# Performance work log

Hardware: AMD Instinct MI355X
Metric: run time of the kernel (lower is better)

The kernel has to match this reference:

```python
import jax, jax.numpy as jnp
import numpy as np

N_TOTAL = 200000
DIM = 256
N_GRAPHS = 8192
N_ITERS = 6


def setup_inputs() -> dict:
    key = jax.random.key(0)
    k1, k2, k3, k4, k5, k6 = jax.random.split(key, 6)
    x = jax.random.normal(k1, (N_TOTAL, DIM), dtype=jnp.float32)
    batch = jnp.sort(jax.random.randint(k2, (N_TOTAL,), 0, N_GRAPHS)).astype(jnp.int32)
    bound = 1.0 / np.sqrt(DIM)
    W_ih = jax.random.uniform(k3, (4 * DIM, DIM), jnp.float32, -bound, bound)
    W_hh = jax.random.uniform(k4, (4 * DIM, DIM), jnp.float32, -bound, bound)
    b_ih = jax.random.uniform(k5, (4 * DIM,), jnp.float32, -bound, bound)
    b_hh = jax.random.uniform(k6, (4 * DIM,), jnp.float32, -bound, bound)
    return {"x": x, "batch": batch, "n_graphs": N_GRAPHS,
            "W_ih": W_ih, "W_hh": W_hh, "b_ih": b_ih, "b_hh": b_hh}


def _lstm_cell(inp, h, c, W_ih, W_hh, b_ih, b_hh):
    # PyTorch LSTMCell: gates ordered i, f, g, o
    gates = inp @ W_ih.T + b_ih + h @ W_hh.T + b_hh
    i, f, g, o = jnp.split(gates, 4, axis=-1)
    c_new = jax.nn.sigmoid(f) * c + jax.nn.sigmoid(i) * jnp.tanh(g)
    h_new = jax.nn.sigmoid(o) * jnp.tanh(c_new)
    return h_new, c_new


def reference(x, batch, n_graphs, W_ih, W_hh, b_ih, b_hh):
    dim = x.shape[1]
    h = jnp.zeros((n_graphs, dim), x.dtype)
    c = jnp.zeros((n_graphs, dim), x.dtype)
    readout = jnp.zeros((n_graphs, dim), x.dtype)
    for _ in range(N_ITERS):
        # attention scores per node: <x_v, q_{g(v)}>
        scores = jnp.sum(x * h[batch], axis=-1)  # (N,)
        # torch scatter_reduce_ amax with zero init includes the 0 -> max(seg_max, 0)
        seg_max = jax.ops.segment_max(scores, batch, num_segments=n_graphs,
                                      indices_are_sorted=True)
        seg_max = jnp.maximum(seg_max, 0.0)
        e = jnp.exp(scores - seg_max[batch])
        seg_sum = jax.ops.segment_sum(e, batch, num_segments=n_graphs,
                                      indices_are_sorted=True)
        w = e / (seg_sum[batch] + 1e-8)  # (N,)
        readout = jax.ops.segment_sum(x * w[:, None], batch, num_segments=n_graphs,
                                      indices_are_sorted=True)  # (G, dim)
        h, c = _lstm_cell(readout, h, c, W_ih, W_hh, b_ih, b_hh)
    return jnp.concatenate([h, readout], axis=-1)  # (G, 2*dim)
```

## Files before the change

### kernel.cpp

```cpp
#include <hip/hip_runtime.h>
#include <hip/hip_bf16.h>
#include <hip/hip_fp16.h>
#include <stdint.h>

#define DIM 256
#define NG 8192
#define KDIM 512
#define GDIM 1024
#define N_ITERS 6
#define CHUNK 32

#define BM 128
#define BN 128
#define BK 64

typedef __hip_bfloat16 bf16;
typedef __attribute__((ext_vector_type(8))) short bf16x8;
typedef __attribute__((ext_vector_type(4))) float f32x4;
typedef __attribute__((ext_vector_type(8))) unsigned short u16x8;
typedef __attribute__((ext_vector_type(4))) unsigned short u16x4;

__device__ __forceinline__ void async16(void* lds, const void* g) {
    __builtin_amdgcn_global_load_lds((const __attribute__((address_space(1))) void*)g,
                                     (__attribute__((address_space(3))) void*)lds, 16, 0, 0);
}
__device__ __forceinline__ float fast_sigmoid(float v) {
    return 1.0f / (1.0f + __expf(-v));
}
__device__ __forceinline__ float fast_tanh(float v) {
    float e = __expf(2.0f * v);
    return (e - 1.0f) / (e + 1.0f);
}
__device__ __forceinline__ unsigned short f2bf(float v) {
    __hip_bfloat16 t = __float2bfloat16(v);
    unsigned short u; __builtin_memcpy(&u, &t, 2); return u;
}
__device__ __forceinline__ unsigned short f2h(float v) {
    __half t = __float2half_rn(v);
    unsigned short u; __builtin_memcpy(&u, &t, 2); return u;
}
__device__ __forceinline__ float h2f(unsigned short u) {
    __half t; __builtin_memcpy(&t, &u, 2);
    return __half2float(t);
}

__global__ void k_offsets(const int* __restrict__ batch, int* __restrict__ offs, int n_nodes) {
    int v = blockIdx.x * blockDim.x + threadIdx.x;
    if (v >= n_nodes) return;
    int b = batch[v];
    int bp = (v == 0) ? -1 : batch[v - 1];
    for (int g = bp + 1; g <= b; ++g) offs[g] = v;
    if (v == n_nodes - 1) {
        for (int g = b + 1; g <= NG; ++g) offs[g] = n_nodes;
    }
}

__global__ void k_prep_w(const float* __restrict__ Wih, const float* __restrict__ Whh,
                         const float* __restrict__ bih, const float* __restrict__ bhh,
                         bf16* __restrict__ Wcat, float* __restrict__ bsum) {
    int idx = blockIdx.x * blockDim.x + threadIdx.x;
    if (idx < GDIM * KDIM) {
        int n = idx >> 9;
        int k = idx & (KDIM - 1);
        int d = n >> 2, gate = n & 3;
        int j = gate * DIM + d;
        float v = (k < DIM) ? Wih[j * DIM + k] : Whh[j * DIM + (k - DIM)];
        Wcat[idx] = __float2bfloat16(v);
    }
    if (idx < GDIM) {
        int d = idx >> 2, gate = idx & 3;
        int j = gate * DIM + d;
        bsum[idx] = bih[j] + bhh[j];
    }
}

__global__ void k_zero(float* __restrict__ h, float* __restrict__ c, bf16* __restrict__ Acat0) {
    int i = blockIdx.x * blockDim.x + threadIdx.x;
    if (i >= NG * DIM) return;
    h[i] = 0.0f; c[i] = 0.0f;
    Acat0[(size_t)(i >> 8) * KDIM + DIM + (i & 255)] = __float2bfloat16(0.0f);
}

template <bool FIRST>
__global__ __launch_bounds__(256) void k_att(const float* __restrict__ xf,
                                             unsigned short* __restrict__ xb,
                                             const float* __restrict__ h,
                                             const int* __restrict__ offs,
                                             float* __restrict__ readout,
                                             bf16* __restrict__ AcatOut) {
    const int g = blockIdx.x;
    const int tid = threadIdx.x;
    const int wave = tid >> 6, lane = tid & 63;
    const int sub = lane >> 5, hl = lane & 31;

    __shared__ unsigned short xs[CHUNK][DIM];
    __shared__ float sc[CHUNK];
    __shared__ float esh[CHUNK];

    float hreg[8];
    {
        const float4 h0 = *(const float4*)&h[(size_t)g * DIM + hl * 8];
        const float4 h1 = *(const float4*)&h[(size_t)g * DIM + hl * 8 + 4];
        hreg[0] = h0.x; hreg[1] = h0.y; hreg[2] = h0.z; hreg[3] = h0.w;
        hreg[4] = h1.x; hreg[5] = h1.y; hreg[6] = h1.z; hreg[7] = h1.w;
    }

    const int start = offs[g], end = offs[g + 1];
    float racc = 0.0f;
    float m = 0.0f;
    float s = 0.0f;

    for (int base = start; base < end; base += CHUNK) {
        const int cnt = min(CHUNK, end - base);
        for (int i = wave * 2; i < cnt; i += 8) {
            const int r = i + sub;
            if (r < cnt) {
                u16x8 pk;
                float dt = 0.0f;
                if (FIRST) {
                    const float4 a = *(const float4*)&xf[(size_t)(base + r) * DIM + hl * 8];
                    const float4 b = *(const float4*)&xf[(size_t)(base + r) * DIM + hl * 8 + 4];
                    float xv[8] = {a.x, a.y, a.z, a.w, b.x, b.y, b.z, b.w};
                    #pragma unroll
                    for (int j = 0; j < 8; ++j) { pk[j] = f2h(xv[j]); dt = fmaf(xv[j], hreg[j], dt); }
                    *(u16x8*)&xb[(size_t)(base + r) * DIM + hl * 8] = pk;
                } else {
                    pk = *(const u16x8*)&xb[(size_t)(base + r) * DIM + hl * 8];
                    #pragma unroll
                    for (int j = 0; j < 8; ++j) dt = fmaf(h2f(pk[j]), hreg[j], dt);
                }
                *(u16x8*)&xs[r][hl * 8] = pk;
                #pragma unroll
                for (int off = 16; off > 0; off >>= 1) dt += __shfl_xor(dt, off);
                if (hl == 0) sc[r] = dt;
            }
        }
        __syncthreads();
        float cmax = m;
        for (int i = 0; i < cnt; ++i) cmax = fmaxf(cmax, sc[i]);
        const float alpha = __expf(m - cmax);
        racc *= alpha;
        s *= alpha;
        if (tid < cnt) esh[tid] = __expf(sc[tid] - cmax);
        m = cmax;
        __syncthreads();
        for (int i = 0; i < cnt; ++i) {
            const float e = esh[i];
            s += e;
            racc = fmaf(e, h2f(xs[i][tid]), racc);
        }
        __syncthreads();
    }

    const float out = racc / (s + 1e-8f);
    readout[(size_t)g * DIM + tid] = out;
    AcatOut[(size_t)g * KDIM + tid] = __float2bfloat16(out);
}

__global__ __launch_bounds__(256) void k_gemm_cell(const bf16* __restrict__ A,
                                                   const bf16* __restrict__ W,
                                                   const float* __restrict__ bsum,
                                                   float* __restrict__ cst,
                                                   float* __restrict__ hst,
                                                   bf16* __restrict__ AcatN) {
    __shared__ union {
        struct { bf16 As[BM * BK]; bf16 Bs[BN * BK]; } st;
        float ep[32][132];
    } sm;

    const int tid = threadIdx.x;
    const int wave = tid >> 6, lane = tid & 63;
    const int m0 = blockIdx.x * BM;
    const int n0 = blockIdx.y * BN;
    const int wr = wave >> 1, wc = wave & 1;

    f32x4 acc[4][4] = {};

    const int chunk = lane & 7;

    for (int k0 = 0; k0 < KDIM; k0 += BK) {
        #pragma unroll
        for (int i = 0; i < 4; ++i) {
            const int grp = wave * 32 + i * 8;
            async16(&sm.st.As[grp * BK],
                    A + (size_t)(m0 + grp + (lane >> 3)) * KDIM + k0 + chunk * 8);
        }
        #pragma unroll
        for (int i = 0; i < 4; ++i) {
            const int grp = wave * 32 + i * 8;
            async16(&sm.st.Bs[grp * BK],
                    W + (size_t)(n0 + grp + (lane >> 3)) * KDIM + k0 + chunk * 8);
        }
        asm volatile("s_waitcnt vmcnt(0)" ::: "memory");
        __syncthreads();

        #pragma unroll
        for (int ks = 0; ks < BK; ks += 32) {
            bf16x8 a[4], b[4];
            #pragma unroll
            for (int mi = 0; mi < 4; ++mi)
                a[mi] = *(const bf16x8*)&sm.st.As[(wr * 64 + mi * 16 + (lane & 15)) * BK + ks + (lane >> 4) * 8];
            #pragma unroll
            for (int ni = 0; ni < 4; ++ni)
                b[ni] = *(const bf16x8*)&sm.st.Bs[(wc * 64 + ni * 16 + (lane & 15)) * BK + ks + (lane >> 4) * 8];
            #pragma unroll
            for (int mi = 0; mi < 4; ++mi)
                #pragma unroll
                for (int ni = 0; ni < 4; ++ni)
                    acc[mi][ni] = __builtin_amdgcn_mfma_f32_16x16x32_bf16(a[mi], b[ni], acc[mi][ni], 0, 0, 0);
        }
        __syncthreads();
    }

    float bv[4];
    #pragma unroll
    for (int ni = 0; ni < 4; ++ni)
        bv[ni] = bsum[n0 + wc * 64 + ni * 16 + (lane & 15)];

    const int d0 = n0 >> 2;
    const int lr = tid >> 3;
    const int dd = (tid & 7) * 4;

    #pragma unroll
    for (int mi = 0; mi < 4; ++mi) {
        __syncthreads();
        #pragma unroll
        for (int ni = 0; ni < 4; ++ni) {
            const int colL = wc * 64 + ni * 16 + (lane & 15);
            #pragma unroll
            for (int r = 0; r < 4; ++r) {
                const int lrow = wr * 16 + (lane >> 4) * 4 + r;
                sm.ep[lrow][colL] = acc[mi][ni][r] + bv[ni];
            }
        }
        __syncthreads();
        const int grow = m0 + (lr >> 4) * 64 + mi * 16 + (lr & 15);
        const int d = d0 + dd;
        float co[4], cn[4], hn[4];
        *(float4*)co = *(const float4*)&cst[(size_t)grow * DIM + d];
        u16x4 hb;
        #pragma unroll
        for (int j = 0; j < 4; ++j) {
            const float4 q = *(const float4*)&sm.ep[lr][(dd + j) * 4];
            cn[j] = fast_sigmoid(q.y) * co[j] + fast_sigmoid(q.x) * fast_tanh(q.z);
            hn[j] = fast_sigmoid(q.w) * fast_tanh(cn[j]);
            hb[j] = f2bf(hn[j]);
        }
        *(float4*)&cst[(size_t)grow * DIM + d] = *(float4*)cn;
        *(float4*)&hst[(size_t)grow * DIM + d] = *(float4*)hn;
        *(u16x4*)&AcatN[(size_t)grow * KDIM + DIM + d] = hb;
    }
}

__global__ void k_out(const float* __restrict__ h, const float* __restrict__ readout,
                      float* __restrict__ out) {
    int idx = blockIdx.x * blockDim.x + threadIdx.x;
    if (idx >= NG * KDIM) return;
    const int g = idx >> 9, d = idx & (KDIM - 1);
    out[idx] = (d < DIM) ? h[(size_t)g * DIM + d] : readout[(size_t)g * DIM + (d - DIM)];
}

extern "C" void kernel_launch(void* const* d_in, const int* in_sizes, int n_in,
                              void* d_out, int out_size, void* d_ws, size_t ws_size,
                              hipStream_t stream) {
    const float* x     = (const float*)d_in[0];
    const int*   batch = (const int*)d_in[1];
    const float* Wih   = (const float*)d_in[3];
    const float* Whh   = (const float*)d_in[4];
    const float* bih   = (const float*)d_in[5];
    const float* bhh   = (const float*)d_in[6];
    const int n_nodes  = in_sizes[0] / DIM;
    float* out = (float*)d_out;

    char* ws = (char*)d_ws;
    size_t off = 0;
    auto alloc = [&](size_t bytes) -> void* {
        off = (off + 255) & ~(size_t)255;
        void* p = ws + off;
        off += bytes;
        return p;
    };
    int*   offs    = (int*)  alloc((size_t)(NG + 1) * sizeof(int));
    bf16*  Wcat    = (bf16*) alloc((size_t)GDIM * KDIM * sizeof(bf16));
    float* bsum    = (float*)alloc((size_t)GDIM * sizeof(float));
    bf16*  Acat0   = (bf16*) alloc((size_t)NG * KDIM * sizeof(bf16));
    bf16*  Acat1   = (bf16*) alloc((size_t)NG * KDIM * sizeof(bf16));
    float* h       = (float*)alloc((size_t)NG * DIM * sizeof(float));
    float* c       = (float*)alloc((size_t)NG * DIM * sizeof(float));
    float* readout = (float*)alloc((size_t)NG * DIM * sizeof(float));
    unsigned short* xb = (unsigned short*)alloc((size_t)n_nodes * DIM * sizeof(unsigned short));
    (void)ws_size; (void)n_in; (void)out_size;

    k_offsets<<<(n_nodes + 255) / 256, 256, 0, stream>>>(batch, offs, n_nodes);
    k_prep_w<<<(GDIM * KDIM + 255) / 256, 256, 0, stream>>>(Wih, Whh, bih, bhh, Wcat, bsum);
    k_zero<<<(NG * DIM + 255) / 256, 256, 0, stream>>>(h, c, Acat0);

    for (int it = 0; it < N_ITERS; ++it) {
        bf16* Ain  = (it & 1) ? Acat1 : Acat0;
        bf16* Aout = (it & 1) ? Acat0 : Acat1;
        if (it == 0)
            k_att<true><<<NG, 256, 0, stream>>>(x, xb, h, offs, readout, Ain);
        else
            k_att<false><<<NG, 256, 0, stream>>>(x, xb, h, offs, readout, Ain);
        k_gemm_cell<<<dim3(NG / BM, GDIM / BN), 256, 0, stream>>>(Ain, Wcat, bsum, c, h, Aout);
    }
    k_out<<<(NG * KDIM + 255) / 256, 256, 0, stream>>>(h, readout, out);
}
```

Before: 883.9 us.

## Use one wave per graph with online softmax and fuse setup/output kernels

The attention kernel now assigns one wavefront per graph instead of a 256-thread block. Each half-wave processes alternate nodes with a streaming online softmax kept in registers, then the two halves merge with cross-lane shuffles. This removes the shared-memory staging and the block barriers. The three setup kernels are merged into one, and the final iteration writes h and readout straight into the output so the separate concat kernel goes away. The per-wave loop is serial over nodes, so graphs with many nodes could load-balance less well.

Result: faster. 832.5 us (-5.8%).

```diff
diff --git a/kernel.cpp b/kernel.cpp
--- a/kernel.cpp
+++ b/kernel.cpp
@@ -8,7 +8,6 @@
 #define KDIM 512
 #define GDIM 1024
 #define N_ITERS 6
-#define CHUNK 32
 
 #define BM 128
 #define BN 128
@@ -44,125 +43,132 @@
     return __half2float(t);
 }
 
-__global__ void k_offsets(const int* __restrict__ batch, int* __restrict__ offs, int n_nodes) {
-    int v = blockIdx.x * blockDim.x + threadIdx.x;
-    if (v >= n_nodes) return;
-    int b = batch[v];
-    int bp = (v == 0) ? -1 : batch[v - 1];
-    for (int g = bp + 1; g <= b; ++g) offs[g] = v;
-    if (v == n_nodes - 1) {
-        for (int g = b + 1; g <= NG; ++g) offs[g] = n_nodes;
-    }
-}
-
-__global__ void k_prep_w(const float* __restrict__ Wih, const float* __restrict__ Whh,
-                         const float* __restrict__ bih, const float* __restrict__ bhh,
-                         bf16* __restrict__ Wcat, float* __restrict__ bsum) {
-    int idx = blockIdx.x * blockDim.x + threadIdx.x;
+__global__ void k_prep(const int* __restrict__ batch, int n_nodes, int* __restrict__ offs,
+                       const float* __restrict__ Wih, const float* __restrict__ Whh,
+                       const float* __restrict__ bih, const float* __restrict__ bhh,
+                       bf16* __restrict__ Wcat, float* __restrict__ bsum,
+                       float* __restrict__ h, float* __restrict__ c, bf16* __restrict__ Acat0) {
+    const int idx = blockIdx.x * blockDim.x + threadIdx.x;
+    if (idx < NG * DIM) {
+        h[idx] = 0.0f; c[idx] = 0.0f;
+        Acat0[(size_t)(idx >> 8) * KDIM + DIM + (idx & 255)] = __float2bfloat16(0.0f);
+    }
     if (idx < GDIM * KDIM) {
-        int n = idx >> 9;
-        int k = idx & (KDIM - 1);
-        int d = n >> 2, gate = n & 3;
-        int j = gate * DIM + d;
-        float v = (k < DIM) ? Wih[j * DIM + k] : Whh[j * DIM + (k - DIM)];
+        const int n = idx >> 9;
+        const int k = idx & (KDIM - 1);
+        const int d = n >> 2, gate = n & 3;
+        const int j = gate * DIM + d;
+        const float v = (k < DIM) ? Wih[j * DIM + k] : Whh[j * DIM + (k - DIM)];
         Wcat[idx] = __float2bfloat16(v);
     }
     if (idx < GDIM) {
-        int d = idx >> 2, gate = idx & 3;
-        int j = gate * DIM + d;
+        const int d = idx >> 2, gate = idx & 3;
+        const int j = gate * DIM + d;
         bsum[idx] = bih[j] + bhh[j];
     }
-}
-
-__global__ void k_zero(float* __restrict__ h, float* __restrict__ c, bf16* __restrict__ Acat0) {
-    int i = blockIdx.x * blockDim.x + threadIdx.x;
-    if (i >= NG * DIM) return;
-    h[i] = 0.0f; c[i] = 0.0f;
-    Acat0[(size_t)(i >> 8) * KDIM + DIM + (i & 255)] = __float2bfloat16(0.0f);
-}
-
-template <bool FIRST>
+    if (idx < n_nodes) {
+        const int b = batch[idx];
+        const int bp = (idx == 0) ? -1 : batch[idx - 1];
+        for (int g = bp + 1; g <= b; ++g) offs[g] = idx;
+        if (idx == n_nodes - 1)
+            for (int g = b + 1; g <= NG; ++g) offs[g] = n_nodes;
+    }
+}
+
+template <bool FIRST, bool LAST>
 __global__ __launch_bounds__(256) void k_att(const float* __restrict__ xf,
                                              unsigned short* __restrict__ xb,
                                              const float* __restrict__ h,
                                              const int* __restrict__ offs,
-                                             float* __restrict__ readout,
+                                             float* __restrict__ rout,
                                              bf16* __restrict__ AcatOut) {
-    const int g = blockIdx.x;
-    const int tid = threadIdx.x;
-    const int wave = tid >> 6, lane = tid & 63;
-    const int sub = lane >> 5, hl = lane & 31;
-
-    __shared__ unsigned short xs[CHUNK][DIM];
-    __shared__ float sc[CHUNK];
-    __shared__ float esh[CHUNK];
+    const int wave = threadIdx.x >> 6;
+    const int g = (blockIdx.x << 2) + wave;
+    const int lane = threadIdx.x & 63;
+    const int half = lane >> 5, hl = lane & 31;
 
     float hreg[8];
     {
-        const float4 h0 = *(const float4*)&h[(size_t)g * DIM + hl * 8];
-        const float4 h1 = *(const float4*)&h[(size_t)g * DIM + hl * 8 + 4];
-        hreg[0] = h0.x; hreg[1] = h0.y; hreg[2] = h0.z; hreg[3] = h0.w;
-        hreg[4] = h1.x; hreg[5] = h1.y; hreg[6] = h1.z; hreg[7] = h1.w;
+        const float4 a = *(const float4*)&h[(size_t)g * DIM + hl * 8];
+        const float4 b = *(const float4*)&h[(size_t)g * DIM + hl * 8 + 4];
+        hreg[0] = a.x; hreg[1] = a.y; hreg[2] = a.z; hreg[3] = a.w;
+        hreg[4] = b.x; hreg[5] = b.y; hreg[6] = b.z; hreg[7] = b.w;
     }
 
     const int start = offs[g], end = offs[g + 1];
-    float racc = 0.0f;
+    float racc[8] = {0, 0, 0, 0, 0, 0, 0, 0};
     float m = 0.0f;
     float s = 0.0f;
 
-    for (int base = start; base < end; base += CHUNK) {
-        const int cnt = min(CHUNK, end - base);
-        for (int i = wave * 2; i < cnt; i += 8) {
-            const int r = i + sub;
-            if (r < cnt) {
+    for (int r0 = start; r0 < end; r0 += 2) {
+        const int r = r0 + half;
+        const bool valid = (r < end);
+        float xv[8];
+        float dt = 0.0f;
+        if (valid) {
+            if (FIRST) {
+                const float4 a = *(const float4*)&xf[(size_t)r * DIM + hl * 8];
+                const float4 b = *(const float4*)&xf[(size_t)r * DIM + hl * 8 + 4];
+                xv[0] = a.x; xv[1] = a.y; xv[2] = a.z; xv[3] = a.w;
+                xv[4] = b.x; xv[5] = b.y; xv[6] = b.z; xv[7] = b.w;
                 u16x8 pk;
-                float dt = 0.0f;
-                if (FIRST) {
-                    const float4 a = *(const float4*)&xf[(size_t)(base + r) * DIM + hl * 8];
-                    const float4 b = *(const float4*)&xf[(size_t)(base + r) * DIM + hl * 8 + 4];
-                    float xv[8] = {a.x, a.y, a.z, a.w, b.x, b.y, b.z, b.w};
-                    #pragma unroll
-                    for (int j = 0; j < 8; ++j) { pk[j] = f2h(xv[j]); dt = fmaf(xv[j], hreg[j], dt); }
-                    *(u16x8*)&xb[(size_t)(base + r) * DIM + hl * 8] = pk;
-                } else {
-                    pk = *(const u16x8*)&xb[(size_t)(base + r) * DIM + hl * 8];
-                    #pragma unroll
-                    for (int j = 0; j < 8; ++j) dt = fmaf(h2f(pk[j]), hreg[j], dt);
-                }
-                *(u16x8*)&xs[r][hl * 8] = pk;
                 #pragma unroll
-                for (int off = 16; off > 0; off >>= 1) dt += __shfl_xor(dt, off);
-                if (hl == 0) sc[r] = dt;
+                for (int j = 0; j < 8; ++j) pk[j] = f2h(xv[j]);
+                *(u16x8*)&xb[(size_t)r * DIM + hl * 8] = pk;
+            } else {
+                const u16x8 pk = *(const u16x8*)&xb[(size_t)r * DIM + hl * 8];
+                #pragma unroll
+                for (int j = 0; j < 8; ++j) xv[j] = h2f(pk[j]);
             }
-        }
-        __syncthreads();
-        float cmax = m;
-        for (int i = 0; i < cnt; ++i) cmax = fmaxf(cmax, sc[i]);
-        const float alpha = __expf(m - cmax);
-        racc *= alpha;
-        s *= alpha;
-        if (tid < cnt) esh[tid] = __expf(sc[tid] - cmax);
-        m = cmax;
-        __syncthreads();
-        for (int i = 0; i < cnt; ++i) {
-            const float e = esh[i];
-            s += e;
-            racc = fmaf(e, h2f(xs[i][tid]), racc);
-        }
-        __syncthreads();
-    }
-
-    const float out = racc / (s + 1e-8f);
-    readout[(size_t)g * DIM + tid] = out;
-    AcatOut[(size_t)g * KDIM + tid] = __float2bfloat16(out);
-}
-
+            #pragma unroll
+            for (int j = 0; j < 8; ++j) dt = fmaf(xv[j], hreg[j], dt);
+        }
+        #pragma unroll
+        for (int off = 16; off > 0; off >>= 1) dt += __shfl_xor(dt, off);
+        if (valid) {
+            const float mn = fmaxf(m, dt);
+            const float al = __expf(m - mn);
+            const float e  = __expf(dt - mn);
+            s = s * al + e;
+            #pragma unroll
+            for (int j = 0; j < 8; ++j) racc[j] = fmaf(racc[j], al, e * xv[j]);
+            m = mn;
+        }
+    }
+
+    const float mo = __shfl_xor(m, 32);
+    const float M  = fmaxf(m, mo);
+    const float al = __expf(m - M);
+    s *= al;
+    #pragma unroll
+    for (int j = 0; j < 8; ++j) racc[j] *= al;
+    s += __shfl_xor(s, 32);
+    #pragma unroll
+    for (int j = 0; j < 8; ++j) racc[j] += __shfl_xor(racc[j], 32);
+    const float inv = 1.0f / (s + 1e-8f);
+    float o[8];
+    #pragma unroll
+    for (int j = 0; j < 8; ++j) o[j] = racc[j] * inv;
+
+    if (half == 0) {
+        u16x8 pk;
+        #pragma unroll
+        for (int j = 0; j < 8; ++j) pk[j] = f2bf(o[j]);
+        *(u16x8*)&AcatOut[(size_t)g * KDIM + hl * 8] = pk;
+    } else if (LAST) {
+        *(float4*)&rout[(size_t)g * KDIM + hl * 8]     = make_float4(o[0], o[1], o[2], o[3]);
+        *(float4*)&rout[(size_t)g * KDIM + hl * 8 + 4] = make_float4(o[4], o[5], o[6], o[7]);
+    }
+}
+
+template <bool LAST>
 __global__ __launch_bounds__(256) void k_gemm_cell(const bf16* __restrict__ A,
                                                    const bf16* __restrict__ W,
                                                    const float* __restrict__ bsum,
                                                    float* __restrict__ cst,
                                                    float* __restrict__ hst,
-                                                   bf16* __restrict__ AcatN) {
+                                                   bf16* __restrict__ AcatN,
+                                                   float* __restrict__ hout) {
     __shared__ union {
         struct { bf16 As[BM * BK]; bf16 Bs[BN * BK]; } st;
         float ep[32][132];
@@ -175,7 +181,6 @@
     const int wr = wave >> 1, wc = wave & 1;
 
     f32x4 acc[4][4] = {};
-
     const int chunk = lane & 7;
 
     for (int k0 = 0; k0 < KDIM; k0 += BK) {
@@ -246,18 +251,14 @@
             hn[j] = fast_sigmoid(q.w) * fast_tanh(cn[j]);
             hb[j] = f2bf(hn[j]);
         }
-        *(float4*)&cst[(size_t)grow * DIM + d] = *(float4*)cn;
-        *(float4*)&hst[(size_t)grow * DIM + d] = *(float4*)hn;
-        *(u16x4*)&AcatN[(size_t)grow * KDIM + DIM + d] = hb;
-    }
-}
-
-__global__ void k_out(const float* __restrict__ h, const float* __restrict__ readout,
-                      float* __restrict__ out) {
-    int idx = blockIdx.x * blockDim.x + threadIdx.x;
-    if (idx >= NG * KDIM) return;
-    const int g = idx >> 9, d = idx & (KDIM - 1);
-    out[idx] = (d < DIM) ? h[(size_t)g * DIM + d] : readout[(size_t)g * DIM + (d - DIM)];
+        if (LAST) {
+            *(float4*)&hout[(size_t)grow * KDIM + d] = *(float4*)hn;
+        } else {
+            *(float4*)&cst[(size_t)grow * DIM + d] = *(float4*)cn;
+            *(float4*)&hst[(size_t)grow * DIM + d] = *(float4*)hn;
+            *(u16x4*)&AcatN[(size_t)grow * KDIM + DIM + d] = hb;
+        }
+    }
 }
 
 extern "C" void kernel_launch(void* const* d_in, const int* in_sizes, int n_in,
@@ -280,29 +281,34 @@
         off += bytes;
         return p;
     };
-    int*   offs    = (int*)  alloc((size_t)(NG + 1) * sizeof(int));
-    bf16*  Wcat    = (bf16*) alloc((size_t)GDIM * KDIM * sizeof(bf16));
-    float* bsum    = (float*)alloc((size_t)GDIM * sizeof(float));
-    bf16*  Acat0   = (bf16*) alloc((size_t)NG * KDIM * sizeof(bf16));
-    bf16*  Acat1   = (bf16*) alloc((size_t)NG * KDIM * sizeof(bf16));
-    float* h       = (float*)alloc((size_t)NG * DIM * sizeof(float));
-    float* c       = (float*)alloc((size_t)NG * DIM * sizeof(float));
-    float* readout = (float*)alloc((size_t)NG * DIM * sizeof(float));
+    int*   offs  = (int*)  alloc((size_t)(NG + 1) * sizeof(int));
+    bf16*  Wcat  = (bf16*) alloc((size_t)GDIM * KDIM * sizeof(bf16));
+    float* bsum  = (float*)alloc((size_t)GDIM * sizeof(float));
+    bf16*  Acat0 = (bf16*) alloc((size_t)NG * KDIM * sizeof(bf16));
+    bf16*  Acat1 = (bf16*) alloc((size_t)NG * KDIM * sizeof(bf16));
+    float* h     = (float*)alloc((size_t)NG * DIM * sizeof(float));
+    float* c     = (float*)alloc((size_t)NG * DIM * sizeof(float));
     unsigned short* xb = (unsigned short*)alloc((size_t)n_nodes * DIM * sizeof(unsigned short));
     (void)ws_size; (void)n_in; (void)out_size;
 
-    k_offsets<<<(n_nodes + 255) / 256, 256, 0, stream>>>(batch, offs, n_nodes);
-    k_prep_w<<<(GDIM * KDIM + 255) / 256, 256, 0, stream>>>(Wih, Whh, bih, bhh, Wcat, bsum);
-    k_zero<<<(NG * DIM + 255) / 256, 256, 0, stream>>>(h, c, Acat0);
+    k_prep<<<NG * DIM / 256, 256, 0, stream>>>(batch, n_nodes, offs, Wih, Whh, bih, bhh,
+                                               Wcat, bsum, h, c, Acat0);
 
     for (int it = 0; it < N_ITERS; ++it) {
         bf16* Ain  = (it & 1) ? Acat1 : Acat0;
         bf16* Aout = (it & 1) ? Acat0 : Acat1;
         if (it == 0)
-            k_att<true><<<NG, 256, 0, stream>>>(x, xb, h, offs, readout, Ain);
+            k_att<true, false><<<NG / 4, 256, 0, stream>>>(x, xb, h, offs, nullptr, Ain);
+        else if (it < N_ITERS - 1)
+            k_att<false, false><<<NG / 4, 256, 0, stream>>>(x, xb, h, offs, nullptr, Ain);
         else
-            k_att<false><<<NG, 256, 0, stream>>>(x, xb, h, offs, readout, Ain);
-        k_gemm_cell<<<dim3(NG / BM, GDIM / BN), 256, 0, stream>>>(Ain, Wcat, bsum, c, h, Aout);
-    }
-    k_out<<<(NG * KDIM + 255) / 256, 256, 0, stream>>>(h, readout, out);
-}
+            k_att<false, true><<<NG / 4, 256, 0, stream>>>(x, xb, h, offs, out + DIM, Ain);
+
+        if (it < N_ITERS - 1)
+            k_gemm_cell<false><<<dim3(NG / BM, GDIM / BN), 256, 0, stream>>>(
+                Ain, Wcat, bsum, c, h, Aout, nullptr);
+        else
+            k_gemm_cell<true><<<dim3(NG / BM, GDIM / BN), 256, 0, stream>>>(
+                Ain, Wcat, bsum, c, nullptr, nullptr, out);
+    }
+}
```
